# Optimization experiments

Hardware: AMD Instinct MI355X
Metric: run time of the kernel (lower is better)

Reference implementation:

```python
import jax, jax.numpy as jnp
import numpy as np

SIZE = 512              # LocallyConnected1D kernel size
B, L, C = 16, 1534, 16  # L = 3*SIZE - 2 so residual broadcast is valid
O1 = L - SIZE + 1       # 1023, length after elu_dense
O2 = O1 - SIZE + 1      # 512, length after linear_dense
EPS = 1e-3              # keras BatchNormalization default epsilon


def _local_matmul(x, W, b):
    """LocallyConnected1D(filters=1, kernel=SIZE, valid): unshared per-position weights.
    x: [B, Lin, Cin]; W: [Lout, SIZE, Cin]; b: [Lout] -> returns [B, Lout]."""
    Lout = W.shape[0]
    idx = jnp.arange(Lout)[:, None] + jnp.arange(SIZE)[None, :]   # [Lout, SIZE]
    patches = x[:, idx, :]                                        # [B, Lout, SIZE, Cin]
    return jnp.einsum('bosc,osc->bo', patches, W) + b[None, :]


def setup_inputs() -> dict:
    key = jax.random.key(0)
    ks = jax.random.split(key, 12)
    x  = jax.random.normal(ks[0], (B, L, C), jnp.float32)
    W1 = jax.random.normal(ks[1], (O1, SIZE, C), jnp.float32) * (1.0 / np.sqrt(SIZE * C))
    b1 = jax.random.normal(ks[2], (O1,), jnp.float32) * 0.01
    W2 = jax.random.normal(ks[3], (O2, SIZE, 1), jnp.float32) * (1.0 / np.sqrt(SIZE))
    b2 = jax.random.normal(ks[4], (O2,), jnp.float32) * 0.01
    Wl = jax.random.normal(ks[5], (1, SIZE, 1), jnp.float32) * (1.0 / np.sqrt(SIZE))
    bl = jax.random.normal(ks[6], (1,), jnp.float32) * 0.01
    Ws = jax.random.normal(ks[7], (1, SIZE, 1), jnp.float32) * (1.0 / np.sqrt(SIZE))
    bs = jax.random.normal(ks[8], (1,), jnp.float32) * 0.01
    gamma = 1.0 + 0.1 * jax.random.normal(ks[9], (C,), jnp.float32)
    beta  = 0.1 * jax.random.normal(ks[10], (C,), jnp.float32)
    mov_mean = 0.1 * jax.random.normal(ks[11], (C,), jnp.float32)
    mov_var  = jnp.ones((C,), jnp.float32)
    return dict(x=x, W1=W1, b1=b1, W2=W2, b2=b2, Wl=Wl, bl=bl, Ws=Ws, bs=bs,
                gamma=gamma, beta=beta, mov_mean=mov_mean, mov_var=mov_var)


def reference(x, W1, b1, W2, b2, Wl, bl, Ws, bs, gamma, beta, mov_mean, mov_var):
    # elu_dense: LocallyConnected1D(1, size, activation='elu')
    h1 = jax.nn.elu(_local_matmul(x, W1, b1))[..., None]          # [B, O1, 1]
    # linear_dense (dropout is identity at inference)
    h2 = _local_matmul(h1, W2, b2)[..., None]                     # [B, O2, 1]
    # gated linear unit: linear * sigmoid, each a LocallyConnected1D with out_len 1
    lin = _local_matmul(h2, Wl, bl)                               # [B, 1]
    sig = jax.nn.sigmoid(_local_matmul(h2, Ws, bs))               # [B, 1]
    g = (lin * sig)[..., None]                                    # [B, 1, 1]
    # residual: zero-padded input + broadcast GLU output
    xp = jnp.pad(x, ((0, 0), (0, 1), (0, 0)))                     # [B, L+1, C]
    y = xp + g                                                    # broadcast over length & channels
    # BatchNormalization (inference): per-channel affine normalize
    return (y - mov_mean) * jax.lax.rsqrt(mov_var + EPS) * gamma + beta
```

## Files before the change

### kernel.cpp

```cpp
#include <hip/hip_runtime.h>
#include <math.h>

namespace {
constexpr int B_ = 16;
constexpr int L_ = 1534;
constexpr int LC = L_ * 16;
constexpr int O1 = 1023;
constexpr int K_ = 8192;
constexpr int KSPLIT = 8;
constexpr int KQ = K_ / KSPLIT;
constexpr int KC = 256;
constexpr int OUTL = 1535;
constexpr float EPS = 1e-3f;
constexpr int XS_F4 = 112;
constexpr int WS_F4 = 80;
constexpr int H1P_FLOATS = KSPLIT * B_ * O1;
}

__global__ __launch_bounds__(512, 4) void k_h1(const float* __restrict__ x,
                                               const float* __restrict__ W1,
                                               float* __restrict__ h1p,
                                               float* __restrict__ gacc) {
  __shared__ float4 xs[16 * XS_F4];
  __shared__ float4 wsld[16 * WS_F4];

  const int tile = (int)blockIdx.x >> 3;
  const int split = (int)blockIdx.x & 7;
  const int o0 = tile * 16;
  const int q0 = split * KQ;
  const int t = (int)threadIdx.x;
  const int bgrp = t >> 8;
  const int ogrp = (t >> 6) & 3;
  const int ks = t & 63;

  float acc[4][8];
#pragma unroll
  for (int j = 0; j < 4; ++j)
#pragma unroll
    for (int i = 0; i < 8; ++i) acc[j][i] = 0.f;

  const int nc = (split == KSPLIT - 1) ? 5 : 4;
  for (int c = 0; c < nc; ++c) {
    const int qc = q0 + c * KC;

#pragma unroll
    for (int i = 0; i < 3; ++i) {
      const int idx = t + i * 512;
      if (idx < 16 * WS_F4) {
        const int ol = idx / WS_F4;
        const int f4 = idx - ol * WS_F4;
        const int q = qc - 48 + f4 * 4;
        const int o = o0 + ol;
        float4 v = make_float4(0.f, 0.f, 0.f, 0.f);
        if (o < O1 && q >= 0 && q <= K_ - 4)
          v = *(const float4*)(W1 + o * K_ + q);
        wsld[idx] = v;
      }
    }
#pragma unroll
    for (int i = 0; i < 4; ++i) {
      const int idx = t + i * 512;
      if (idx < 16 * XS_F4) {
        const int b = idx / XS_F4;
        const int f4 = idx - b * XS_F4;
        const int p = o0 * 16 + qc + f4 * 4;
        float4 v = make_float4(0.f, 0.f, 0.f, 0.f);
        if (p <= LC - 4) v = *(const float4*)(x + b * LC + p);
        xs[idx] = v;
      }
    }
    __syncthreads();

    float4 wv[4];
#pragma unroll
    for (int jj = 0; jj < 4; ++jj)
      wv[jj] = wsld[(ogrp * 4 + jj) * WS_F4 + (ks - 4 * jj + 12)];
    float4 xv[8];
#pragma unroll
    for (int bi = 0; bi < 8; ++bi)
      xv[bi] = xs[(bgrp * 8 + bi) * XS_F4 + (ogrp * 16 + ks)];
#pragma unroll
    for (int jj = 0; jj < 4; ++jj)
#pragma unroll
      for (int bi = 0; bi < 8; ++bi) {
        acc[jj][bi] = fmaf(xv[bi].x, wv[jj].x, acc[jj][bi]);
        acc[jj][bi] = fmaf(xv[bi].y, wv[jj].y, acc[jj][bi]);
        acc[jj][bi] = fmaf(xv[bi].z, wv[jj].z, acc[jj][bi]);
        acc[jj][bi] = fmaf(xv[bi].w, wv[jj].w, acc[jj][bi]);
      }
    __syncthreads();
  }

  float* redf = (float*)xs;
  float4* red4 = xs;
  const int cls = bgrp * 4 + ogrp;
#pragma unroll
  for (int r = 0; r < 4; ++r) {
    __syncthreads();
    red4[(cls * 64 + ks) * 2 + 0] =
        make_float4(acc[r][0], acc[r][1], acc[r][2], acc[r][3]);
    red4[(cls * 64 + ks) * 2 + 1] =
        make_float4(acc[r][4], acc[r][5], acc[r][6], acc[r][7]);
    __syncthreads();
    const int out = t >> 3;
    const int seg = t & 7;
    const int rcls = out >> 3, bi = out & 7;
    float v = 0.f;
#pragma unroll
    for (int j = 0; j < 8; ++j)
      v += redf[(rcls * 64 + seg * 8 + j) * 8 + bi];
    v += __shfl_xor(v, 1, 64);
    v += __shfl_xor(v, 2, 64);
    v += __shfl_xor(v, 4, 64);
    if (seg == 0) {
      const int b = (rcls >> 2) * 8 + bi;
      const int o = o0 + (rcls & 3) * 4 + r;
      if (o < O1) h1p[(split * B_ + b) * O1 + o] = v;
    }
  }
  if (blockIdx.x == 0 && t < 32) gacc[t] = 0.f;
}

__global__ __launch_bounds__(256) void k_h2(const float* __restrict__ h1p,
                                            const float* __restrict__ b1,
                                            const float* __restrict__ W2,
                                            const float* __restrict__ b2,
                                            const float* __restrict__ Wl,
                                            const float* __restrict__ Wsg,
                                            float* __restrict__ gacc) {
  const int bid = (int)blockIdx.x;
  const int b = bid >> 3;
  const int tile = bid & 7;
  const int base = tile * 64;
  const int t = (int)threadIdx.x;
  const int wave = t >> 6;
  const int lane = t & 63;

  __shared__ float hw[575];
  for (int i = t; i < 575; i += 256) {
    const int o = base + i;
    float v = b1[o];
#pragma unroll
    for (int s = 0; s < KSPLIT; ++s) v += h1p[(s * B_ + b) * O1 + o];
    hw[i] = v > 0.f ? v : expm1f(v);
  }
  __syncthreads();

  float lin_acc = 0.f, sig_acc = 0.f;
  for (int i = wave; i < 64; i += 4) {
    const int o2 = base + i;
    const float4 wa = *(const float4*)(W2 + o2 * 512 + lane * 4);
    const float4 wb = *(const float4*)(W2 + o2 * 512 + 256 + lane * 4);
    const int sa = i + lane * 4;
    float a = 0.f;
    a = fmaf(hw[sa + 0], wa.x, a);
    a = fmaf(hw[sa + 1], wa.y, a);
    a = fmaf(hw[sa + 2], wa.z, a);
    a = fmaf(hw[sa + 3], wa.w, a);
    a = fmaf(hw[sa + 256], wb.x, a);
    a = fmaf(hw[sa + 257], wb.y, a);
    a = fmaf(hw[sa + 258], wb.z, a);
    a = fmaf(hw[sa + 259], wb.w, a);
#pragma unroll
    for (int off = 32; off >= 1; off >>= 1) a += __shfl_xor(a, off, 64);
    const float h2 = a + b2[o2];
    lin_acc = fmaf(h2, Wl[o2], lin_acc);
    sig_acc = fmaf(h2, Wsg[o2], sig_acc);
  }

  __shared__ float lred[4], sred[4];
  if (lane == 0) { lred[wave] = lin_acc; sred[wave] = sig_acc; }
  __syncthreads();
  if (t == 0) {
    atomicAdd(&gacc[b], lred[0] + lred[1] + lred[2] + lred[3]);
    atomicAdd(&gacc[16 + b], sred[0] + sred[1] + sred[2] + sred[3]);
  }
}

__global__ __launch_bounds__(256) void k_out(const float* __restrict__ x,
                                             const float* __restrict__ gacc,
                                             const float* __restrict__ bl,
                                             const float* __restrict__ bs,
                                             const float* __restrict__ gamma,
                                             const float* __restrict__ beta,
                                             const float* __restrict__ mmean,
                                             const float* __restrict__ mvar,
                                             float* __restrict__ out) {
  const int f4 = blockIdx.x * 256 + (int)threadIdx.x;
  if (f4 >= B_ * OUTL * 4) return;
  const int b = f4 / (OUTL * 4);
  const int q = f4 - b * (OUTL * 4);
  const int l = q >> 2;
  const int c0 = (q & 3) * 4;

  const float lin = gacc[b] + bl[0];
  const float sv = gacc[16 + b] + bs[0];
  const float g = lin * (1.f / (1.f + expf(-sv)));

  float4 xin = make_float4(0.f, 0.f, 0.f, 0.f);
  if (l < L_) xin = *(const float4*)(x + b * LC + l * 16 + c0);

  const float4 gm = *(const float4*)(gamma + c0);
  const float4 bt = *(const float4*)(beta + c0);
  const float4 mm = *(const float4*)(mmean + c0);
  const float4 mv = *(const float4*)(mvar + c0);

  float4 r;
  r.x = (xin.x + g - mm.x) * (rsqrtf(mv.x + EPS) * gm.x) + bt.x;
  r.y = (xin.y + g - mm.y) * (rsqrtf(mv.y + EPS) * gm.y) + bt.y;
  r.z = (xin.z + g - mm.z) * (rsqrtf(mv.z + EPS) * gm.z) + bt.z;
  r.w = (xin.w + g - mm.w) * (rsqrtf(mv.w + EPS) * gm.w) + bt.w;
  *(float4*)(out + f4 * 4) = r;
}

extern "C" void kernel_launch(void* const* d_in, const int* in_sizes, int n_in,
                              void* d_out, int out_size, void* d_ws, size_t ws_size,
                              hipStream_t stream) {
  const float* x    = (const float*)d_in[0];
  const float* W1   = (const float*)d_in[1];
  const float* b1   = (const float*)d_in[2];
  const float* W2   = (const float*)d_in[3];
  const float* b2   = (const float*)d_in[4];
  const float* Wl   = (const float*)d_in[5];
  const float* bl   = (const float*)d_in[6];
  const float* Wsg  = (const float*)d_in[7];
  const float* bs   = (const float*)d_in[8];
  const float* gm   = (const float*)d_in[9];
  const float* bt   = (const float*)d_in[10];
  const float* mmn  = (const float*)d_in[11];
  const float* mvr  = (const float*)d_in[12];

  float* ws   = (float*)d_ws;
  float* h1p  = ws;
  float* gacc = ws + H1P_FLOATS;

  k_h1<<<512, 512, 0, stream>>>(x, W1, h1p, gacc);
  k_h2<<<128, 256, 0, stream>>>(h1p, b1, W2, b2, Wl, Wsg, gacc);
  k_out<<<(B_ * OUTL * 4 + 255) / 256, 256, 0, stream>>>(
      x, gacc, bl, bs, gm, bt, mmn, mvr, (float*)d_out);
}
```

Baseline: 126.9 us.

## Use ring-buffered shared tiles with register prefetch in k_h1

Replaces the per-chunk full reload of the x and W1 tiles with 128-entry circular shared-memory buffers. Only the new 64 float4s per row are loaded for each chunk, so the overlapping halo is no longer re-read. The next chunk's global loads are issued into registers before the current chunk's FMAs, which overlaps memory latency with compute. The cost is extra registers for the prefetch, larger shared buffers that may lower occupancy, and more complex modular indexing that must stay correct.

```diff
diff --git a/kernel.cpp b/kernel.cpp
--- a/kernel.cpp
+++ b/kernel.cpp
@@ -9,11 +9,8 @@
 constexpr int K_ = 8192;
 constexpr int KSPLIT = 8;
 constexpr int KQ = K_ / KSPLIT;
-constexpr int KC = 256;
 constexpr int OUTL = 1535;
 constexpr float EPS = 1e-3f;
-constexpr int XS_F4 = 112;
-constexpr int WS_F4 = 80;
 constexpr int H1P_FLOATS = KSPLIT * B_ * O1;
 }
 
@@ -21,8 +18,8 @@
                                                const float* __restrict__ W1,
                                                float* __restrict__ h1p,
                                                float* __restrict__ gacc) {
-  __shared__ float4 xs[16 * XS_F4];
-  __shared__ float4 wsld[16 * WS_F4];
+  __shared__ float4 xs[16 * 128];
+  __shared__ float4 wsh[16 * 128];
 
   const int tile = (int)blockIdx.x >> 3;
   const int split = (int)blockIdx.x & 7;
@@ -32,63 +29,81 @@
   const int bgrp = t >> 8;
   const int ogrp = (t >> 6) & 3;
   const int ks = t & 63;
+  const int wv_ = t >> 6;
+  const int lane = t & 63;
+
+  const float4 z4 = make_float4(0.f, 0.f, 0.f, 0.f);
+
+  for (int i = 0; i < 4; ++i) {
+    const int idx = t + i * 512;
+    const int row = idx >> 7;
+    const int s = idx & 127;
+    if (s < 112) {
+      const int p = o0 * 16 + q0 + 4 * s;
+      float4 v = z4;
+      if (p <= LC - 4) v = *(const float4*)(x + row * LC + p);
+      xs[row * 128 + s] = v;
+    }
+    if (s < 76) {
+      const int q = q0 + 4 * (s - 12);
+      const int o = o0 + row;
+      float4 v = z4;
+      if (o < O1 && q >= 0 && q <= K_ - 4) v = *(const float4*)(W1 + o * K_ + q);
+      wsh[row * 128 + ((s - 12) & 127)] = v;
+    }
+  }
 
   float acc[4][8];
 #pragma unroll
   for (int j = 0; j < 4; ++j)
 #pragma unroll
     for (int i = 0; i < 8; ++i) acc[j][i] = 0.f;
+
+  float4 px[2], pw[2];
+
+  __syncthreads();
 
   const int nc = (split == KSPLIT - 1) ? 5 : 4;
   for (int c = 0; c < nc; ++c) {
-    const int qc = q0 + c * KC;
-
-#pragma unroll
-    for (int i = 0; i < 3; ++i) {
-      const int idx = t + i * 512;
-      if (idx < 16 * WS_F4) {
-        const int ol = idx / WS_F4;
-        const int f4 = idx - ol * WS_F4;
-        const int q = qc - 48 + f4 * 4;
-        const int o = o0 + ol;
-        float4 v = make_float4(0.f, 0.f, 0.f, 0.f);
-        if (o < O1 && q >= 0 && q <= K_ - 4)
-          v = *(const float4*)(W1 + o * K_ + q);
-        wsld[idx] = v;
+    if (c > 0) {
+      __syncthreads();
+#pragma unroll
+      for (int h = 0; h < 2; ++h) {
+        const int row = h * 8 + wv_;
+        xs[row * 128 + ((48 + c * 64 + lane) & 127)] = px[h];
+        wsh[row * 128 + ((c * 64 + lane) & 127)] = pw[h];
       }
-    }
-#pragma unroll
-    for (int i = 0; i < 4; ++i) {
-      const int idx = t + i * 512;
-      if (idx < 16 * XS_F4) {
-        const int b = idx / XS_F4;
-        const int f4 = idx - b * XS_F4;
-        const int p = o0 * 16 + qc + f4 * 4;
-        float4 v = make_float4(0.f, 0.f, 0.f, 0.f);
-        if (p <= LC - 4) v = *(const float4*)(x + b * LC + p);
-        xs[idx] = v;
+      __syncthreads();
+    }
+    if (c + 1 < nc) {
+      const int cc = c + 1;
+#pragma unroll
+      for (int h = 0; h < 2; ++h) {
+        const int row = h * 8 + wv_;
+        const int p = o0 * 16 + q0 + 448 + c * 256 + 4 * lane;
+        px[h] = (p <= LC - 4) ? *(const float4*)(x + row * LC + p) : z4;
+        const int q = q0 + cc * 256 + 4 * lane;
+        const int o = o0 + row;
+        pw[h] = (o < O1 && q <= K_ - 4) ? *(const float4*)(W1 + o * K_ + q) : z4;
       }
     }
-    __syncthreads();
-
-    float4 wv[4];
+    float4 wvv[4];
 #pragma unroll
     for (int jj = 0; jj < 4; ++jj)
-      wv[jj] = wsld[(ogrp * 4 + jj) * WS_F4 + (ks - 4 * jj + 12)];
+      wvv[jj] = wsh[(ogrp * 4 + jj) * 128 + ((c * 64 + ks - 4 * jj) & 127)];
     float4 xv[8];
 #pragma unroll
     for (int bi = 0; bi < 8; ++bi)
-      xv[bi] = xs[(bgrp * 8 + bi) * XS_F4 + (ogrp * 16 + ks)];
+      xv[bi] = xs[(bgrp * 8 + bi) * 128 + ((c * 64 + ogrp * 16 + ks) & 127)];
 #pragma unroll
     for (int jj = 0; jj < 4; ++jj)
 #pragma unroll
       for (int bi = 0; bi < 8; ++bi) {
-        acc[jj][bi] = fmaf(xv[bi].x, wv[jj].x, acc[jj][bi]);
-        acc[jj][bi] = fmaf(xv[bi].y, wv[jj].y, acc[jj][bi]);
-        acc[jj][bi] = fmaf(xv[bi].z, wv[jj].z, acc[jj][bi]);
-        acc[jj][bi] = fmaf(xv[bi].w, wv[jj].w, acc[jj][bi]);
+        acc[jj][bi] = fmaf(xv[bi].x, wvv[jj].x, acc[jj][bi]);
+        acc[jj][bi] = fmaf(xv[bi].y, wvv[jj].y, acc[jj][bi]);
+        acc[jj][bi] = fmaf(xv[bi].z, wvv[jj].z, acc[jj][bi]);
+        acc[jj][bi] = fmaf(xv[bi].w, wvv[jj].w, acc[jj][bi]);
       }
-    __syncthreads();
   }
 
   float* redf = (float*)xs;
```

After: 155.8 us. 1.23x slower.
